# Kernel optimization log

Measured on AMD Instinct MI355X. Metric: run time of the kernel, lower is better.

## Reference

```python
import jax, jax.numpy as jnp
import numpy as np

N_EXPERTS = 8
TOP_K = 2
D_MODEL = 1024
D_FF = 4 * D_MODEL

def setup_inputs() -> dict:
    key = jax.random.key(0)
    ks = jax.random.split(key, 5)
    s_in = 1.0 / np.sqrt(D_MODEL)
    s_ff = 1.0 / np.sqrt(D_FF)
    return {
        "x": jax.random.normal(ks[0], (2, 2048, D_MODEL), dtype=jnp.float32),
        "Wr": jax.random.normal(ks[1], (N_EXPERTS, D_MODEL), dtype=jnp.float32) * s_in,
        "W1": jax.random.normal(ks[2], (N_EXPERTS, D_FF, D_MODEL), dtype=jnp.float32) * s_in,
        "W2": jax.random.normal(ks[3], (N_EXPERTS, D_MODEL, D_FF), dtype=jnp.float32) * s_ff,
        "W3": jax.random.normal(ks[4], (N_EXPERTS, D_FF, D_MODEL), dtype=jnp.float32) * s_in,
    }

def reference(x, Wr, W1, W2, W3):
    B, S, D = x.shape
    T = B * S
    xf = x.reshape(T, D)
    logits = xf @ Wr.T                         # [T, E]
    probs = jax.nn.softmax(logits, axis=-1)
    top_p, top_i = jax.lax.top_k(probs, TOP_K)  # [T, K]
    top_p = top_p / jnp.sum(top_p, axis=-1, keepdims=True)
    # per-token combine weight for each expert: [T, E]
    onehot = jax.nn.one_hot(top_i, N_EXPERTS, dtype=x.dtype)  # [T, K, E]
    cw = jnp.einsum('tke,tk->te', onehot, top_p)
    out = jnp.zeros_like(xf)
    for e in range(N_EXPERTS):  # fixed small structural loop over experts
        h = jax.nn.silu(xf @ W1[e].T) * (xf @ W3[e].T)  # [T, F]
        y = h @ W2[e].T                                 # [T, D]
        out = out + cw[:, e:e+1] * y
    importance = jnp.sum(probs, axis=0)                 # [E]
    load = jnp.sum(jnp.sum(onehot, axis=1), axis=0)     # [E]
    aux_loss = jnp.sum(importance * load) * (N_EXPERTS / (T ** 2 + 1e-06))
    return out.reshape(B, S, D), aux_loss
```

## Files before the change

### kernel.cpp

```cpp
#include <hip/hip_runtime.h>

#define T_TOK 4096
#define DM 1024
#define DF 4096
#define NE 8
#define BM 256
#define RCAP 10240
#define MAXT 40
#define MAXT2 80
#define ACH_B 32768
#define CHUNK_B 8192

typedef _Float16 f16x8 __attribute__((ext_vector_type(8)));
typedef float f32x4 __attribute__((ext_vector_type(4)));

#define MFMA16(a, b, c) __builtin_amdgcn_mfma_f32_16x16x32_f16(a, b, c, 0, 0, 0)
#define RAW_BAR() __builtin_amdgcn_s_barrier()
#define VMCNT(n) asm volatile("s_waitcnt vmcnt(" #n ")" ::: "memory")

__device__ __forceinline__ ushort f2h_bits(float f) {
    _Float16 h = (_Float16)f;
    return __builtin_bit_cast(unsigned short, h);
}

__device__ __forceinline__ unsigned int pk2(float a, float b) {
    return __builtin_bit_cast(unsigned int, __builtin_amdgcn_cvt_pkrtz(a, b));
}

__device__ __forceinline__ uint4 pack8f(float4 a, float4 b) {
    uint4 r;
    r.x = pk2(a.x, a.y); r.y = pk2(a.z, a.w);
    r.z = pk2(b.x, b.y); r.w = pk2(b.z, b.w);
    return r;
}

__device__ __forceinline__ void gll16(const void* g, void* l) {
    __builtin_amdgcn_global_load_lds(
        (const __attribute__((address_space(1))) unsigned int*)g,
        (__attribute__((address_space(3))) unsigned int*)l, 16, 0, 0);
}

__global__ __launch_bounds__(256) void k_init(float* __restrict__ out,
                                              int* __restrict__ misc,
                                              int* __restrict__ row_tok) {
    int i = blockIdx.x * 256 + threadIdx.x;
    if (i < T_TOK * DM + 1) out[i] = 0.f;
    if (i < RCAP) row_tok[i] = -1;
    if (i < 256) misc[i] = 0;
}

__global__ __launch_bounds__(64) void k_router(const float* __restrict__ x,
                                               const float* __restrict__ Wr,
                                               float* __restrict__ probs,
                                               int* __restrict__ topi,
                                               float* __restrict__ topw,
                                               int* __restrict__ cnt) {
    int t = blockIdx.x;
    int lane = threadIdx.x;
    const float* xr = x + (size_t)t * DM;
    float s[NE];
#pragma unroll
    for (int e = 0; e < NE; e++) s[e] = 0.f;
    for (int j = lane; j < DM; j += 64) {
        float xv = xr[j];
#pragma unroll
        for (int e = 0; e < NE; e++) s[e] += xv * Wr[e * DM + j];
    }
#pragma unroll
    for (int off = 32; off > 0; off >>= 1) {
#pragma unroll
        for (int e = 0; e < NE; e++) s[e] += __shfl_xor(s[e], off, 64);
    }
    if (lane == 0) {
        float mx = s[0];
#pragma unroll
        for (int e = 1; e < NE; e++) mx = fmaxf(mx, s[e]);
        float ex[NE], sum = 0.f;
#pragma unroll
        for (int e = 0; e < NE; e++) { ex[e] = expf(s[e] - mx); sum += ex[e]; }
        float inv = 1.f / sum;
        float p[NE];
#pragma unroll
        for (int e = 0; e < NE; e++) { p[e] = ex[e] * inv; probs[t * NE + e] = p[e]; }
        int i0 = 0;
#pragma unroll
        for (int e = 1; e < NE; e++) if (p[e] > p[i0]) i0 = e;
        int i1 = (i0 == 0) ? 1 : 0;
#pragma unroll
        for (int e = 0; e < NE; e++) if (e != i0 && p[e] > p[i1]) i1 = e;
        float w0 = p[i0], w1 = p[i1], winv = 1.f / (w0 + w1);
        topi[2 * t] = i0;     topw[2 * t] = w0 * winv;
        topi[2 * t + 1] = i1; topw[2 * t + 1] = w1 * winv;
        atomicAdd(&cnt[i0], 1);
        atomicAdd(&cnt[i1], 1);
    }
}

__global__ __launch_bounds__(256) void k_scan(const float* __restrict__ probs,
                                              const int* __restrict__ cnt,
                                              int* __restrict__ poff,
                                              int* __restrict__ texp,
                                              int* __restrict__ texp2,
                                              int* __restrict__ ntp,
                                              float* __restrict__ aux_out) {
    __shared__ float red[256 * NE];
    int tid = threadIdx.x;
    float part[NE];
#pragma unroll
    for (int e = 0; e < NE; e++) part[e] = 0.f;
    for (int t = tid; t < T_TOK; t += 256) {
#pragma unroll
        for (int e = 0; e < NE; e++) part[e] += probs[t * NE + e];
    }
#pragma unroll
    for (int e = 0; e < NE; e++) red[tid * NE + e] = part[e];
    __syncthreads();
    for (int s2 = 128; s2 > 0; s2 >>= 1) {
        if (tid < s2) {
#pragma unroll
            for (int e = 0; e < NE; e++) red[tid * NE + e] += red[(tid + s2) * NE + e];
        }
        __syncthreads();
    }
    if (tid == 0) {
        float al = 0.f;
#pragma unroll
        for (int e = 0; e < NE; e++) al += red[e] * (float)cnt[e];
        *aux_out = al * (8.0f / (16777216.0f + 1e-6f));
        int run = 0, tix = 0;
        for (int e = 0; e < NE; e++) {
            poff[e] = run;
            int nt = (cnt[e] + BM - 1) / BM;
            for (int i = 0; i < nt; i++) texp[tix++] = e;
            run += nt * BM;
        }
        ntp[0] = run / BM;
        ntp[1] = run / 128;
        for (int j = 0; j < MAXT2; j++) texp2[j] = (j >> 1) < tix ? texp[j >> 1] : 0;
    }
}

__global__ __launch_bounds__(256) void k_assign(const int* __restrict__ topi,
                                                const float* __restrict__ topw,
                                                const int* __restrict__ poff,
                                                int* __restrict__ fill,
                                                int* __restrict__ row_tok,
                                                float* __restrict__ row_w) {
    int t = blockIdx.x * 256 + threadIdx.x;
    if (t >= T_TOK) return;
#pragma unroll
    for (int k = 0; k < 2; k++) {
        int e = topi[2 * t + k];
        int pos = atomicAdd(&fill[e], 1);
        int r = poff[e] + pos;
        row_tok[r] = t;
        row_w[r] = topw[2 * t + k];
    }
}

__global__ __launch_bounds__(256) void k_convert(const float* __restrict__ src,
                                                 ushort* __restrict__ dst,
                                                 int row_len) {
    int nk = row_len >> 6;
    int kt = blockIdx.x, rt = blockIdx.y;
    int tid = threadIdx.x;
    int r = tid >> 2, c0 = (tid & 3) * 16;
    const float* s = src + (size_t)(rt * 64 + r) * row_len + kt * 64 + c0;
    float4 v0 = *(const float4*)(s);
    float4 v1 = *(const float4*)(s + 4);
    float4 v2 = *(const float4*)(s + 8);
    float4 v3 = *(const float4*)(s + 12);
    char* chunk = (char*)dst + ((size_t)rt * nk + kt) * CHUNK_B;
    int sw = (r & 7) << 4;
    *(uint4*)(chunk + r * 128 + ((2 * c0) ^ sw)) = pack8f(v0, v1);
    *(uint4*)(chunk + r * 128 + ((2 * c0 + 16) ^ sw)) = pack8f(v2, v3);
}

__global__ __launch_bounds__(512) void k_gather_t(const float* __restrict__ x,
                                                  const int* __restrict__ row_tok,
                                                  ushort* __restrict__ xg) {
    int kt = blockIdx.x, rt = blockIdx.y;
    int tid = threadIdx.x;
    int r = tid >> 1, c0 = (tid & 1) * 32;
    int tok = row_tok[rt * BM + r];
    char* chunk = (char*)xg + ((size_t)rt * 16 + kt) * ACH_B;
    int sw = (r & 7) << 4;
    if (tok >= 0) {
        const float* s = x + (size_t)tok * DM + kt * 64 + c0;
#pragma unroll
        for (int j = 0; j < 4; j++) {
            float4 va = *(const float4*)(s + j * 8);
            float4 vb = *(const float4*)(s + j * 8 + 4);
            *(uint4*)(chunk + r * 128 + ((c0 * 2 + j * 16) ^ sw)) = pack8f(va, vb);
        }
    } else {
        uint4 z = {0, 0, 0, 0};
#pragma unroll
        for (int j = 0; j < 4; j++)
            *(uint4*)(chunk + r * 128 + ((c0 * 2 + j * 16) ^ sw)) = z;
    }
}

__global__ __launch_bounds__(512, 2) void k_g1(const ushort* __restrict__ xg,
                                               const ushort* __restrict__ W1h,
                                               const ushort* __restrict__ W3h,
                                               const int* __restrict__ texp,
                                               const int* __restrict__ ntp,
                                               ushort* __restrict__ hbuf) {
    __shared__ __align__(16) char lds[131072];
    int b = blockIdx.x;
    int xcd = b & 7, s = b >> 3;
    int rt = (s >> 5) * 8 + ((s >> 2) & 7);
    int ct = xcd * 4 + (s & 3);
    if (rt >= ntp[0]) return;
    int e = texp[rt];
    int tid = threadIdx.x, lane = tid & 63, wv = tid >> 6;
    int wr = wv >> 1, wc = wv & 1;

    const char* Ac  = (const char*)xg + (size_t)rt * 16 * ACH_B;
    const char* B1c = (const char*)W1h + ((size_t)(e * 64 + ct * 2) * 16) * CHUNK_B;
    const char* B3c = (const char*)W3h + ((size_t)(e * 64 + ct * 2) * 16) * CHUNK_B;

    const f32x4 fz = {0.f, 0.f, 0.f, 0.f};
    f32x4 acc1[4][4], acc3[4][4];
#pragma unroll
    for (int m = 0; m < 4; m++)
#pragma unroll
        for (int n = 0; n < 4; n++) { acc1[m][n] = fz; acc3[m][n] = fz; }

    f16x8 af[4], bf[4];
    int kb_base = (lane >> 4) * 16;

#define ST_A(kt_, b_, h_) {                                                        \
        const char* s_ = Ac + (kt_) * ACH_B + (h_) * 16384 + wv * 2048 + lane * 16; \
        char* d_ = lds + (b_) * 65536 + (h_) * 16384 + wv * 2048;                   \
        gll16(s_, d_); gll16(s_ + 1024, d_ + 1024); }
#define ST_B(Bc_, kt_, b_, off_) {                                                          \
        gll16(Bc_ + (kt_) * 8192 + wv * 1024 + lane * 16,                                    \
              lds + (b_) * 65536 + (off_) + wv * 1024);                                      \
        gll16(Bc_ + 131072 + (kt_) * 8192 + wv * 1024 + lane * 16,                           \
              lds + (b_) * 65536 + (off_) + 8192 + wv * 1024); }
#define DS_A(b_, ks_) _Pragma("unroll") for (int m = 0; m < 4; m++) {              \
        int r_ = wr * 64 + m * 16 + (lane & 15);                                   \
        af[m] = *(const f16x8*)(lds + (b_) * 65536 + r_ * 128 +                    \
                                 (((ks_) * 64 + kb_base) ^ ((r_ & 7) << 4))); }
#define DS_B(b_, off_, ks_) _Pragma("unroll") for (int n = 0; n < 4; n++) {        \
        int c_ = wc * 64 + n * 16 + (lane & 15);                                   \
        bf[n] = *(const f16x8*)(lds + (b_) * 65536 + (off_) + c_ * 128 +           \
                                 (((ks_) * 64 + kb_base) ^ ((c_ & 7) << 4))); }
#define MM(accX) _Pragma("unroll") for (int n = 0; n < 4; n++)                     \
        _Pragma("unroll") for (int m = 0; m < 4; m++)                              \
            accX[m][n] = MFMA16(af[m], bf[n], accX[m][n]);

    ST_A(0, 0, 0); ST_A(0, 0, 1); ST_B(B1c, 0, 0, 32768); ST_B(B3c, 0, 0, 49152);
    VMCNT(2);
    RAW_BAR();

    for (int it = 0; it < 8; ++it) {
        int t1 = 2 * it + 1;
        int t2 = 2 * it + 2;
        DS_A(0, 0); DS_B(0, 32768, 0);
        ST_A(t1, 1, 0);
        RAW_BAR();
        __builtin_amdgcn_s_setprio(1); MM(acc1); __builtin_amdgcn_s_setprio(0);
        VMCNT(2);
        RAW_BAR();
        DS_B(0, 49152, 0);
        ST_A(t1, 1, 1);
        RAW_BAR();
        __builtin_amdgcn_s_setprio(1); MM(acc3); __builtin_amdgcn_s_setprio(0);
        RAW_BAR();
        DS_A(0, 1); DS_B(0, 32768, 1);
        ST_B(B1c, t1, 1, 32768);
        RAW_BAR();
        __builtin_amdgcn_s_setprio(1); MM(acc1); __builtin_amdgcn_s_setprio(0);
        RAW_BAR();
        DS_B(0, 49152, 1);
        ST_B(B3c, t1, 1, 49152);
        RAW_BAR();
        __builtin_amdgcn_s_setprio(1); MM(acc3); __builtin_amdgcn_s_setprio(0);
        VMCNT(2);
        RAW_BAR();
        DS_A(1, 0); DS_B(1, 32768, 0);
        if (it < 7) ST_A(t2, 0, 0);
        RAW_BAR();
        __builtin_amdgcn_s_setprio(1); MM(acc1); __builtin_amdgcn_s_setprio(0);
        if (it < 7) { VMCNT(2); } else { VMCNT(0); }
        RAW_BAR();
        DS_B(1, 49152, 0);
        if (it < 7) ST_A(t2, 0, 1);
        RAW_BAR();
        __builtin_amdgcn_s_setprio(1); MM(acc3); __builtin_amdgcn_s_setprio(0);
        RAW_BAR();
        DS_A(1, 1); DS_B(1, 32768, 1);
        if (it < 7) ST_B(B1c, t2, 0, 32768);
        RAW_BAR();
        __builtin_amdgcn_s_setprio(1); MM(acc1); __builtin_amdgcn_s_setprio(0);
        RAW_BAR();
        DS_B(1, 49152, 1);
        if (it < 7) ST_B(B3c, t2, 0, 49152);
        RAW_BAR();
        __builtin_amdgcn_s_setprio(1); MM(acc3); __builtin_amdgcn_s_setprio(0);
        if (it < 7) { VMCNT(2); }
        RAW_BAR();
    }
#undef ST_A
#undef ST_B
#undef DS_A
#undef DS_B
#undef MM

#pragma unroll
    for (int m = 0; m < 4; m++) {
#pragma unroll
        for (int i = 0; i < 4; i++) {
            int rl = wr * 64 + m * 16 + (lane >> 4) * 4 + i;
            int sw = (rl & 7) << 4;
#pragma unroll
            for (int n = 0; n < 4; n++) {
                int fl = wc * 64 + n * 16 + (lane & 15);
                float a1 = acc1[m][n][i], a3 = acc3[m][n][i];
                float h = (a1 / (1.f + expf(-a1))) * a3;
                char* hc = (char*)hbuf + ((size_t)rt * 64 + ct * 2 + (fl >> 6)) * ACH_B;
                *(ushort*)(hc + rl * 128 + ((2 * (fl & 63)) ^ sw)) = f2h_bits(h);
            }
        }
    }
}

__global__ __launch_bounds__(256, 2) void k_g2(const ushort* __restrict__ hbuf,
                                               const ushort* __restrict__ W2h,
                                               const int* __restrict__ texp2,
                                               const int* __restrict__ ntp,
                                               const int* __restrict__ row_tok,
                                               const float* __restrict__ row_w,
                                               float* __restrict__ out) {
    __shared__ __align__(16) char lds[73728];
    int b = blockIdx.x;
    int p = (b & 7) * 160 + (b >> 3);
    int rt2 = p >> 4, ct = p & 15;
    if (rt2 >= ntp[1]) return;
    int e = texp2[rt2];
    int tid = threadIdx.x, lane = tid & 63, wv = tid >> 6;
    int wr = wv >> 1, wc = wv & 1;

    const char* Ac = (const char*)hbuf + ((size_t)(rt2 >> 1) * 64) * ACH_B + (rt2 & 1) * 16384;
    const char* Bc = (const char*)W2h + ((size_t)(e * 16 + ct) * 64) * CHUNK_B;

    const f32x4 fz = {0.f, 0.f, 0.f, 0.f};
    f32x4 acc[4][2];
#pragma unroll
    for (int m = 0; m < 4; m++)
#pragma unroll
        for (int n = 0; n < 2; n++) acc[m][n] = fz;

    f16x8 af[4], bf[2];
    int kb_base = (lane >> 4) * 16;

#define BUF3(t_) (((t_) % 3) * 24576)
#define ST2_A(kt_) {                                                                 \
        const char* s_ = Ac + (size_t)(kt_) * ACH_B + wv * 4096 + lane * 16;         \
        char* d_ = lds + BUF3(kt_) + wv * 4096;                                      \
        gll16(s_, d_); gll16(s_ + 1024, d_ + 1024);                                  \
        gll16(s_ + 2048, d_ + 2048); gll16(s_ + 3072, d_ + 3072); }
#define ST2_B(kt_) {                                                                 \
        const char* s_ = Bc + (size_t)(kt_) * 8192 + wv * 2048 + lane * 16;          \
        char* d_ = lds + BUF3(kt_) + 16384 + wv * 2048;                              \
        gll16(s_, d_); gll16(s_ + 1024, d_ + 1024); }
#define DS2_A(bo_, ks_) _Pragma("unroll") for (int m = 0; m < 4; m++) {              \
        int r_ = wr * 64 + m * 16 + (lane & 15);                                     \
        af[m] = *(const f16x8*)(lds + (bo_) + r_ * 128 +                             \
                                 (((ks_) * 64 + kb_base) ^ ((r_ & 7) << 4))); }
#define DS2_B(bo_, ks_) _Pragma("unroll") for (int n = 0; n < 2; n++) {              \
        int c_ = wc * 32 + n * 16 + (lane & 15);                                     \
        bf[n] = *(const f16x8*)(lds + (bo_) + 16384 + c_ * 128 +                     \
                                 (((ks_) * 64 + kb_base) ^ ((c_ & 7) << 4))); }
#define MM2() _Pragma("unroll") for (int n = 0; n < 2; n++)                          \
        _Pragma("unroll") for (int m = 0; m < 4; m++)                                \
            acc[m][n] = MFMA16(af[m], bf[n], acc[m][n]);

    ST2_A(0); ST2_B(0);
    ST2_A(1); ST2_B(1);
    VMCNT(6);
    RAW_BAR();

    for (int t = 0; t < 64; ++t) {
        int bo = BUF3(t);
        DS2_A(bo, 0); DS2_B(bo, 0);
        if (t < 62) ST2_A(t + 2);
        RAW_BAR();
        __builtin_amdgcn_s_setprio(1); MM2(); __builtin_amdgcn_s_setprio(0);
        RAW_BAR();
        DS2_A(bo, 1); DS2_B(bo, 1);
        if (t < 62) ST2_B(t + 2);
        RAW_BAR();
        __builtin_amdgcn_s_setprio(1); MM2(); __builtin_amdgcn_s_setprio(0);
        if (t < 62) { VMCNT(6); }
        else if (t == 62) { VMCNT(0); }
        RAW_BAR();
    }
#undef BUF3
#undef ST2_A
#undef ST2_B
#undef DS2_A
#undef DS2_B
#undef MM2

#pragma unroll
    for (int m = 0; m < 4; m++) {
#pragma unroll
        for (int i = 0; i < 4; i++) {
            int rr = rt2 * 128 + wr * 64 + m * 16 + (lane >> 4) * 4 + i;
            int tok = row_tok[rr];
            if (tok >= 0) {
                float w = row_w[rr];
                float* orow = out + (size_t)tok * DM + ct * 64 + wc * 32 + (lane & 15);
#pragma unroll
                for (int n = 0; n < 2; n++) atomicAdd(&orow[n * 16], w * acc[m][n][i]);
            }
        }
    }
}

extern "C" void kernel_launch(void* const* d_in, const int* in_sizes, int n_in,
                              void* d_out, int out_size, void* d_ws, size_t ws_size,
                              hipStream_t stream) {
    (void)in_sizes; (void)n_in; (void)out_size; (void)ws_size;
    const float* x  = (const float*)d_in[0];
    const float* Wr = (const float*)d_in[1];
    const float* W1 = (const float*)d_in[2];
    const float* W2 = (const float*)d_in[3];
    const float* W3 = (const float*)d_in[4];
    float* out = (float*)d_out;
    char* ws = (char*)d_ws;

    int* misc  = (int*)ws;
    int* cnt   = misc;
    int* fill  = misc + 8;
    int* poff  = misc + 16;
    int* texp  = misc + 24;
    int* texp2 = misc + 64;
    int* ntp   = misc + 144;
    int*    topi    = (int*)(ws + 1024);
    float*  topw    = (float*)(ws + 33792);
    float*  probs   = (float*)(ws + 66560);
    int*    row_tok = (int*)(ws + 197632);
    float*  row_w   = (float*)(ws + 238592);
    ushort* hbuf    = (ushort*)(ws + 279552);
    ushort* W1h     = (ushort*)(ws + 84165632);
    ushort* W3h     = (ushort*)(ws + 151274496);
    ushort* xg      = (ushort*)(ws + 218383360);
    ushort* W2h     = (ushort*)(ws + 218383360);

    k_init<<<(T_TOK * DM + 1 + 255) / 256, 256, 0, stream>>>(out, misc, row_tok);
    k_router<<<T_TOK, 64, 0, stream>>>(x, Wr, probs, topi, topw, cnt);
    k_scan<<<1, 256, 0, stream>>>(probs, cnt, poff, texp, texp2, ntp, out + (size_t)T_TOK * DM);
    k_assign<<<(T_TOK + 255) / 256, 256, 0, stream>>>(topi, topw, poff, fill, row_tok, row_w);

    k_convert<<<dim3(16, 512), 256, 0, stream>>>(W1, W1h, DM);
    k_convert<<<dim3(16, 512), 256, 0, stream>>>(W3, W3h, DM);
    k_gather_t<<<dim3(16, MAXT), 512, 0, stream>>>(x, row_tok, xg);
    k_g1<<<1280, 512, 0, stream>>>(xg, W1h, W3h, texp, ntp, hbuf);
    k_convert<<<dim3(64, 128), 256, 0, stream>>>(W2, W2h, DF);
    k_g2<<<1280, 256, 0, stream>>>(hbuf, W2h, texp2, ntp, row_tok, row_w, out);
}
```

Before: 634.7 us.

## Widen k_g2 output tile to 128 columns with double-buffered pipeline

```diff
diff --git a/kernel.cpp b/kernel.cpp
--- a/kernel.cpp
+++ b/kernel.cpp
@@ -335,71 +335,70 @@
                                                const int* __restrict__ row_tok,
                                                const float* __restrict__ row_w,
                                                float* __restrict__ out) {
-    __shared__ __align__(16) char lds[73728];
+    __shared__ __align__(16) char lds[65536];
     int b = blockIdx.x;
-    int p = (b & 7) * 160 + (b >> 3);
-    int rt2 = p >> 4, ct = p & 15;
+    int xcd = b & 7, s = b >> 3;
+    int rt2 = (s >> 3) * 8 + xcd;
+    int ct = s & 7;
     if (rt2 >= ntp[1]) return;
     int e = texp2[rt2];
     int tid = threadIdx.x, lane = tid & 63, wv = tid >> 6;
     int wr = wv >> 1, wc = wv & 1;
 
     const char* Ac = (const char*)hbuf + ((size_t)(rt2 >> 1) * 64) * ACH_B + (rt2 & 1) * 16384;
-    const char* Bc = (const char*)W2h + ((size_t)(e * 16 + ct) * 64) * CHUNK_B;
+    const char* Bc = (const char*)W2h + ((size_t)(e * 16 + ct * 2) * 64) * CHUNK_B;
 
     const f32x4 fz = {0.f, 0.f, 0.f, 0.f};
-    f32x4 acc[4][2];
+    f32x4 acc[4][4];
 #pragma unroll
     for (int m = 0; m < 4; m++)
 #pragma unroll
-        for (int n = 0; n < 2; n++) acc[m][n] = fz;
-
-    f16x8 af[4], bf[2];
+        for (int n = 0; n < 4; n++) acc[m][n] = fz;
+
+    f16x8 af[4], bf[4];
     int kb_base = (lane >> 4) * 16;
 
-#define BUF3(t_) (((t_) % 3) * 24576)
-#define ST2_A(kt_) {                                                                 \
+#define ST2_A(kt_, b_) {                                                             \
         const char* s_ = Ac + (size_t)(kt_) * ACH_B + wv * 4096 + lane * 16;         \
-        char* d_ = lds + BUF3(kt_) + wv * 4096;                                      \
+        char* d_ = lds + (b_) * 32768 + wv * 4096;                                   \
         gll16(s_, d_); gll16(s_ + 1024, d_ + 1024);                                  \
         gll16(s_ + 2048, d_ + 2048); gll16(s_ + 3072, d_ + 3072); }
-#define ST2_B(kt_) {                                                                 \
-        const char* s_ = Bc + (size_t)(kt_) * 8192 + wv * 2048 + lane * 16;          \
-        char* d_ = lds + BUF3(kt_) + 16384 + wv * 2048;                              \
-        gll16(s_, d_); gll16(s_ + 1024, d_ + 1024); }
-#define DS2_A(bo_, ks_) _Pragma("unroll") for (int m = 0; m < 4; m++) {              \
+#define ST2_B(kt_, b_) {                                                             \
+        const char* s0_ = Bc + (size_t)(kt_) * 8192 + wv * 2048 + lane * 16;         \
+        char* d0_ = lds + (b_) * 32768 + 16384 + wv * 2048;                          \
+        gll16(s0_, d0_); gll16(s0_ + 1024, d0_ + 1024);                              \
+        const char* s1_ = Bc + 524288 + (size_t)(kt_) * 8192 + wv * 2048 + lane * 16; \
+        char* d1_ = lds + (b_) * 32768 + 24576 + wv * 2048;                          \
+        gll16(s1_, d1_); gll16(s1_ + 1024, d1_ + 1024); }
+#define DS2_A(b_, ks_) _Pragma("unroll") for (int m = 0; m < 4; m++) {               \
         int r_ = wr * 64 + m * 16 + (lane & 15);                                     \
-        af[m] = *(const f16x8*)(lds + (bo_) + r_ * 128 +                             \
+        af[m] = *(const f16x8*)(lds + (b_) * 32768 + r_ * 128 +                      \
                                  (((ks_) * 64 + kb_base) ^ ((r_ & 7) << 4))); }
-#define DS2_B(bo_, ks_) _Pragma("unroll") for (int n = 0; n < 2; n++) {              \
-        int c_ = wc * 32 + n * 16 + (lane & 15);                                     \
-        bf[n] = *(const f16x8*)(lds + (bo_) + 16384 + c_ * 128 +                     \
+#define DS2_B(b_, ks_) _Pragma("unroll") for (int n = 0; n < 4; n++) {               \
+        int c_ = wc * 64 + n * 16 + (lane & 15);                                     \
+        bf[n] = *(const f16x8*)(lds + (b_) * 32768 + 16384 + c_ * 128 +              \
                                  (((ks_) * 64 + kb_base) ^ ((c_ & 7) << 4))); }
-#define MM2() _Pragma("unroll") for (int n = 0; n < 2; n++)                          \
+#define MM2() _Pragma("unroll") for (int n = 0; n < 4; n++)                          \
         _Pragma("unroll") for (int m = 0; m < 4; m++)                                \
             acc[m][n] = MFMA16(af[m], bf[n], acc[m][n]);
 
-    ST2_A(0); ST2_B(0);
-    ST2_A(1); ST2_B(1);
-    VMCNT(6);
+    ST2_A(0, 0); ST2_B(0, 0);
+    VMCNT(0);
     RAW_BAR();
 
     for (int t = 0; t < 64; ++t) {
-        int bo = BUF3(t);
-        DS2_A(bo, 0); DS2_B(bo, 0);
-        if (t < 62) ST2_A(t + 2);
+        int cur = t & 1;
+        DS2_A(cur, 0); DS2_B(cur, 0);
+        if (t < 63) { ST2_A(t + 1, cur ^ 1); ST2_B(t + 1, cur ^ 1); }
         RAW_BAR();
         __builtin_amdgcn_s_setprio(1); MM2(); __builtin_amdgcn_s_setprio(0);
         RAW_BAR();
-        DS2_A(bo, 1); DS2_B(bo, 1);
-        if (t < 62) ST2_B(t + 2);
+        DS2_A(cur, 1); DS2_B(cur, 1);
         RAW_BAR();
         __builtin_amdgcn_s_setprio(1); MM2(); __builtin_amdgcn_s_setprio(0);
-        if (t < 62) { VMCNT(6); }
-        else if (t == 62) { VMCNT(0); }
-        RAW_BAR();
-    }
-#undef BUF3
+        if (t < 63) { VMCNT(0); }
+        RAW_BAR();
+    }
 #undef ST2_A
 #undef ST2_B
 #undef DS2_A
@@ -414,9 +413,9 @@
             int tok = row_tok[rr];
             if (tok >= 0) {
                 float w = row_w[rr];
-                float* orow = out + (size_t)tok * DM + ct * 64 + wc * 32 + (lane & 15);
-#pragma unroll
-                for (int n = 0; n < 2; n++) atomicAdd(&orow[n * 16], w * acc[m][n][i]);
+                float* orow = out + (size_t)tok * DM + ct * 128 + wc * 64 + (lane & 15);
+#pragma unroll
+                for (int n = 0; n < 4; n++) atomicAdd(&orow[n * 16], w * acc[m][n][i]);
             }
         }
     }
@@ -462,5 +461,5 @@
     k_gather_t<<<dim3(16, MAXT), 512, 0, stream>>>(x, row_tok, xg);
     k_g1<<<1280, 512, 0, stream>>>(xg, W1h, W3h, texp, ntp, hbuf);
     k_convert<<<dim3(64, 128), 256, 0, stream>>>(W2, W2h, DF);
-    k_g2<<<1280, 256, 0, stream>>>(hbuf, W2h, texp2, ntp, row_tok, row_w, out);
-}
+    k_g2<<<640, 256, 0, stream>>>(hbuf, W2h, texp2, ntp, row_tok, row_w, out);
+}
```

Result: no change. 638.3 us (+0.6%).
